# Optimization experiments

Measured on AMD Instinct MI355X. Metric: run time of the kernel, lower is better.

## Reference

```python
import jax, jax.numpy as jnp
import numpy as np

B, S, HID = 2, 2048, 4096
NH, D = 32, 128          # heads, head_dim
G, GS = 8, 4             # palu groups, group_size (heads per group)
RK = 256                 # rank per K group (rank_k[i])
RV = 2048                # total V rank
FGD = RV // G            # fused_group_dim = 256
FH = FGD * NH            # fused_hidden_dim = 8192
GD = HID // G            # k group_dim = 512
THETA = 10000.0


def setup_inputs() -> dict:
    key = jax.random.key(0)
    ks = jax.random.split(key, 7)
    hidden_states = jax.random.normal(ks[0], (B, S, HID), jnp.float32)
    causal = jnp.tril(jnp.ones((S, S), bool))
    attention_mask = jnp.broadcast_to(
        jnp.where(causal, 0.0, -1e9).astype(jnp.float32)[None, None], (B, 1, S, S))
    position_ids = jnp.broadcast_to(jnp.arange(S, dtype=jnp.int32)[None], (B, S))
    sc = 0.02
    Wq = sc * jax.random.normal(ks[1], (HID, HID), jnp.float32)
    WVT = sc * jax.random.normal(ks[2], (G * RK, HID), jnp.float32)   # k_proj.VT
    U = sc * jax.random.normal(ks[3], (GD, G * RK), jnp.float32)      # k_proj.U
    Wv = sc * jax.random.normal(ks[4], (RV, HID), jnp.float32)
    Wo = sc * jax.random.normal(ks[5], (HID, FH), jnp.float32)
    return dict(hidden_states=hidden_states, attention_mask=attention_mask,
                position_ids=position_ids, Wq=Wq, WVT=WVT, U=U, Wv=Wv, Wo=Wo)


def _rotate_half(x):
    return jnp.concatenate([-x[..., D // 2:], x[..., :D // 2]], axis=-1)


def reference(hidden_states, attention_mask, position_ids, Wq, WVT, U, Wv, Wo):
    b, q, _ = hidden_states.shape
    # projections
    qs = (hidden_states @ Wq.T).reshape(b, q, NH, D).transpose(0, 2, 1, 3)      # (b,H,q,d)
    k_lat = (hidden_states @ WVT.T).reshape(b, q, G, RK).transpose(0, 2, 1, 3)  # (b,G,q,RK)
    v_lat = (hidden_states @ Wv.T).reshape(b, q, G, FGD).transpose(0, 2, 1, 3)  # (b,G,q,FGD)
    # headwise reconstruction of K: group g latent (RK) -> group_dim (512) via U[:, g-slice]
    Ug = U.reshape(GD, G, RK)
    keys = jnp.einsum('bgsr,dgr->bgsd', k_lat, Ug)                 # (b,G,q,512)
    keys = keys.transpose(0, 2, 1, 3).reshape(b, q, NH, D).transpose(0, 2, 1, 3)  # (b,H,q,d)
    # RoPE
    inv_freq = 1.0 / (THETA ** (jnp.arange(0, D, 2, dtype=jnp.float32) / D))
    freqs = position_ids.astype(jnp.float32)[..., None] * inv_freq            # (b,q,d/2)
    emb = jnp.concatenate([freqs, freqs], axis=-1)
    cos, sin = jnp.cos(emb)[:, None], jnp.sin(emb)[:, None]                   # (b,1,q,d)
    qs = qs * cos + _rotate_half(qs) * sin
    keys = keys * cos + _rotate_half(keys) * sin
    # attention scores + mask + fp32 softmax
    attn = jnp.einsum('bhqd,bhkd->bhqk', qs, keys) / np.sqrt(D).astype(np.float32)
    attn = attn + attention_mask
    attn = jax.nn.softmax(attn.astype(jnp.float32), axis=-1).astype(qs.dtype)
    # PALU fused low-rank V path: exact torch reshape/transpose semantics
    aw = attn.reshape(b, G, q * GS, q)                                        # (b,G,gs*q,kv)
    out = jnp.einsum('bgik,bgkf->bgif', aw, v_lat)                            # (b,G,gs*q,FGD)
    out = out.transpose(0, 2, 1, 3).reshape(b, q, FH)                         # (b,q,8192)
    return out @ Wo.T
```

## Files before the change

### kernel.cpp

```cpp
#include <hip/hip_runtime.h>
#include <hip/hip_bf16.h>

typedef __hip_bfloat16 bf16;
typedef __bf16 bf16x8 __attribute__((ext_vector_type(8)));
typedef float f32x4 __attribute__((ext_vector_type(4)));

#define MFMA16(a, b, c) __builtin_amdgcn_mfma_f32_16x16x32_bf16(a, b, c, 0, 0, 0)

__device__ __forceinline__ void llds16(const bf16* g, bf16* lds) {
  __builtin_amdgcn_global_load_lds(
      (const __attribute__((address_space(1))) unsigned int*)g,
      (__attribute__((address_space(3))) unsigned int*)lds, 16, 0, 0);
}

__device__ __forceinline__ void storeC(float* p, float v) { *p = v; }
__device__ __forceinline__ void storeC(bf16* p, float v) { *p = __float2bfloat16(v); }

__global__ __launch_bounds__(256) void cvt_f2b(const float* __restrict__ in,
                                               bf16* __restrict__ out, int n4) {
  int i = blockIdx.x * 256 + threadIdx.x;
  if (i >= n4) return;
  float4 v = ((const float4*)in)[i];
  union { bf16 h[4]; short4 s; } u;
  u.h[0] = __float2bfloat16(v.x);
  u.h[1] = __float2bfloat16(v.y);
  u.h[2] = __float2bfloat16(v.z);
  u.h[3] = __float2bfloat16(v.w);
  ((short4*)out)[i] = u.s;
}

template <typename OUT_T>
__global__ __launch_bounds__(512, 2) void gemm256(
    const bf16* __restrict__ A, const bf16* __restrict__ B, OUT_T* __restrict__ C,
    int K, int lda, int ldb, int ldc) {
  extern __shared__ bf16 sm[];
  const int t = threadIdx.x, w = t >> 6, l = t & 63;
  const int lane_r = l & 15, quad = l >> 4;
  const int wm = (w >> 2) * 128, wn = (w & 3) * 64;
  const long m0 = (long)blockIdx.y * 256, n0 = (long)blockIdx.x * 256;
  const int r0 = t >> 2;
  const int c0 = (((t & 3) ^ (r0 & 3)) << 3);
  const bf16* As0 = A + (m0 + r0) * lda + c0;
  const bf16* As1 = A + (m0 + r0 + 128) * lda + c0;
  const bf16* Bs0 = B + (n0 + r0) * ldb + c0;
  const bf16* Bs1 = B + (n0 + r0 + 128) * ldb + c0;

#define STAGE(sl, kt)                                   \
  do {                                                  \
    long ko = (long)(kt) * 32;                          \
    bf16* dA = sm + (sl) * 16384;                       \
    bf16* dB = dA + 8192;                               \
    llds16(As0 + ko, dA + t * 8);                       \
    llds16(As1 + ko, dA + (t + 512) * 8);               \
    llds16(Bs0 + ko, dB + t * 8);                       \
    llds16(Bs1 + ko, dB + (t + 512) * 8);               \
  } while (0)

  f32x4 acc[8][4] = {};
  const int KT = K >> 5;
  const int sw = quad ^ (lane_r & 3);

  STAGE(0, 0);
  STAGE(1, 1);
  int sl = 0;
  for (int kt = 0; kt < KT; ++kt) {
    const int pre = KT - 1 - kt;
    if (pre >= 2) {
      int sl2 = sl + 2;
      if (sl2 >= 3) sl2 -= 3;
      STAGE(sl2, kt + 2);
      asm volatile("s_waitcnt vmcnt(8)" ::: "memory");
    } else if (pre == 1) {
      asm volatile("s_waitcnt vmcnt(4)" ::: "memory");
    } else {
      asm volatile("s_waitcnt vmcnt(0)" ::: "memory");
    }
    __builtin_amdgcn_s_barrier();
    __builtin_amdgcn_sched_barrier(0);
    const bf16* Al = sm + sl * 16384;
    const bf16* Bl = Al + 8192;
    bf16x8 af[8], bfr[4];
#pragma unroll
    for (int mt = 0; mt < 8; ++mt)
      af[mt] = *(const bf16x8*)&Al[(wm + mt * 16 + lane_r) * 32 + sw * 8];
#pragma unroll
    for (int nt = 0; nt < 4; ++nt)
      bfr[nt] = *(const bf16x8*)&Bl[(wn + nt * 16 + lane_r) * 32 + sw * 8];
    __builtin_amdgcn_s_setprio(1);
#pragma unroll
    for (int mt = 0; mt < 8; ++mt)
#pragma unroll
      for (int nt = 0; nt < 4; ++nt)
        acc[mt][nt] = MFMA16(af[mt], bfr[nt], acc[mt][nt]);
    __builtin_amdgcn_s_setprio(0);
    __builtin_amdgcn_s_barrier();
    if (++sl == 3) sl = 0;
  }
#undef STAGE

#pragma unroll
  for (int mt = 0; mt < 8; ++mt)
#pragma unroll
    for (int nt = 0; nt < 4; ++nt) {
      long row = m0 + wm + mt * 16 + quad * 4;
      long col = n0 + wn + nt * 16 + lane_r;
#pragma unroll
      for (int r = 0; r < 4; ++r) storeC(&C[(row + r) * ldc + col], acc[mt][nt][r]);
    }
}

template <typename OUT_T>
__global__ __launch_bounds__(256) void gemm_bt(
    const bf16* __restrict__ A, const bf16* __restrict__ B, OUT_T* __restrict__ C,
    int M, int N, int K, int lda, int ldb, int ldc,
    long batchA, long batchB, long batchC) {
  __shared__ alignas(16) bf16 As[128 * 32];
  __shared__ alignas(16) bf16 Bs[128 * 32];
  const int t = threadIdx.x;
  const int w = t >> 6, l = t & 63;
  const int lane_r = l & 15, quad = l >> 4;
  const int wm = (w >> 1) * 64, wn = (w & 1) * 64;
  const long m0 = (long)blockIdx.y * 128, n0 = (long)blockIdx.x * 128;
  A += (long)blockIdx.z * batchA;
  B += (long)blockIdx.z * batchB;
  C += (long)blockIdx.z * batchC;
  const int r0a = t >> 2;
  const int cba = (t & 3) * 8;
  f32x4 acc[4][4] = {};
  for (int k0 = 0; k0 < K; k0 += 32) {
    llds16(A + (m0 + r0a) * lda + k0 + cba, &As[t * 8]);
    llds16(A + (m0 + r0a + 64) * lda + k0 + cba, &As[(t + 256) * 8]);
    llds16(B + (n0 + r0a) * ldb + k0 + cba, &Bs[t * 8]);
    llds16(B + (n0 + r0a + 64) * ldb + k0 + cba, &Bs[(t + 256) * 8]);
    __syncthreads();
    bf16x8 af[4], bfr[4];
#pragma unroll
    for (int mt = 0; mt < 4; ++mt)
      af[mt] = *(const bf16x8*)&As[(wm + mt * 16 + lane_r) * 32 + quad * 8];
#pragma unroll
    for (int nt = 0; nt < 4; ++nt)
      bfr[nt] = *(const bf16x8*)&Bs[(wn + nt * 16 + lane_r) * 32 + quad * 8];
#pragma unroll
    for (int mt = 0; mt < 4; ++mt)
#pragma unroll
      for (int nt = 0; nt < 4; ++nt)
        acc[mt][nt] = MFMA16(af[mt], bfr[nt], acc[mt][nt]);
    __syncthreads();
  }
#pragma unroll
  for (int mt = 0; mt < 4; ++mt)
#pragma unroll
    for (int nt = 0; nt < 4; ++nt) {
      long row = m0 + wm + mt * 16 + quad * 4;
      long col = n0 + wn + nt * 16 + lane_r;
#pragma unroll
      for (int r = 0; r < 4; ++r) storeC(&C[(row + r) * ldc + col], acc[mt][nt][r]);
    }
}

__global__ __launch_bounds__(256) void rope_perm(const bf16* __restrict__ in, int ldin,
                                                 bf16* __restrict__ out,
                                                 const int* __restrict__ pos_ids) {
  int idx = blockIdx.x * 256 + threadIdx.x;
  int d = idx & 63;
  int h = (idx >> 6) & 31;
  int bs = idx >> 11;
  int b = bs >> 11, s = bs & 2047;
  float pos = (float)pos_ids[bs];
  float inv = exp2f(-(float)d * (13.287712379549449f / 64.0f));
  float fr = pos * inv, sn, cs;
  sincosf(fr, &sn, &cs);
  long bi = (long)bs * ldin + h * 128 + d;
  long bo = ((long)(b * 32 + h) * 2048 + s) * 128 + d;
  float x1 = __bfloat162float(in[bi]);
  float x2 = __bfloat162float(in[bi + 64]);
  out[bo] = __float2bfloat16(x1 * cs - x2 * sn);
  out[bo + 64] = __float2bfloat16(x2 * cs + x1 * sn);
}

__global__ __launch_bounds__(256) void transpose_kernel(const bf16* __restrict__ v,
                                                        int ldv,
                                                        bf16* __restrict__ vt) {
  __shared__ bf16 tile[32][33];
  int b = blockIdx.z;
  int c0 = blockIdx.x * 32;
  int r0 = blockIdx.y * 32;
  int tx = threadIdx.x & 31, ty = threadIdx.x >> 5;
#pragma unroll
  for (int p = 0; p < 4; ++p) {
    int r = ty + p * 8;
    tile[r][tx] = v[((long)b * 2048 + r0 + r) * ldv + c0 + tx];
  }
  __syncthreads();
#pragma unroll
  for (int p = 0; p < 4; ++p) {
    int cidx = ty + p * 8;
    int cg = c0 + cidx;
    int g = cg >> 8, d = cg & 255;
    int s = r0 + tx;
    vt[((long)((b * 8 + g) * 64 + (s >> 5))) * 8192 + d * 32 + (s & 31)] = tile[tx][cidx];
  }
}

__global__ __launch_bounds__(512, 2) void attn_kernel(const bf16* __restrict__ Q,
                                                      const bf16* __restrict__ Kg,
                                                      const bf16* __restrict__ Vt,
                                                      bf16* __restrict__ fused) {
  __shared__ alignas(16) bf16 smem[32768];
  const int t = threadIdx.x, w = t >> 6, l = t & 63;
  const int lane_r = l & 15, quad = l >> 4;
  const int L = blockIdx.x;
  const int half = L >> 8, pair = L & 255;
  const int hb = pair >> 2, slot = pair & 3;
  const int qt = half ? slot : (7 - slot);
  const int b = hb >> 5, h = hb & 31;
  const int g = h >> 2, j = h & 3;
  const int q0 = qt * 256;
  const int qr0 = q0 + w * 32;
  const float scale = 0.08838834764831845f;

  const bf16* qbase = Q + ((long)(b * 32 + h) * 2048 + qr0 + lane_r) * 128 + quad * 8;
  bf16x8 qf[2][4];
#pragma unroll
  for (int m = 0; m < 2; ++m)
#pragma unroll
    for (int kd = 0; kd < 4; ++kd)
      qf[m][kd] = *(const bf16x8*)(qbase + m * 2048 + kd * 32);

  f32x4 acc[2][16] = {};
  float m_i[2][4], l_i[2][4];
#pragma unroll
  for (int m = 0; m < 2; ++m)
#pragma unroll
    for (int r = 0; r < 4; ++r) { m_i[m][r] = -1e30f; l_i[m][r] = 0.f; }

  const bf16* Kbase = Kg + (long)(b * 32 + h) * 262144;
  const bf16* Vtg = Vt + (long)(b * 8 + g) * 524288;
  const int kr = t >> 4, ck = (t & 15) ^ (kr & 15);
  const bf16* ksrc = Kbase + kr * 128 + ck * 8;
  const int vrA = t >> 2, cvA = (t & 3) ^ (vrA & 3);
  const int vrB = (t + 512) >> 2, cvB = ((t + 512) & 3) ^ (vrB & 3);
  const bf16* vsrcA = Vtg + vrA * 32 + cvA * 8;
  const bf16* vsrcB = Vtg + vrB * 32 + cvB * 8;

#define STAGE_T(buf, kt)                                                    \
  do {                                                                      \
    llds16(ksrc + (long)(kt) * 4096, &smem[(buf) * 4096 + t * 8]);          \
    llds16(vsrcA + (long)(kt) * 8192, &smem[8192 + (buf) * 8192 + t * 8]);  \
    llds16(vsrcB + (long)(kt) * 8192,                                       \
           &smem[8192 + (buf) * 8192 + (t + 512) * 8]);                     \
  } while (0)

  bf16* Pw = smem + 24576 + w * 1024;
  const int pslot = quad ^ ((lane_r >> 1) & 3);
  const int vslot = quad ^ (lane_r & 3);
  int poff0[4], poff1[4];
  {
    const int hi = lane_r >> 3, lo = lane_r & 7;
#pragma unroll
    for (int r = 0; r < 4; ++r) {
      int rq = quad * 4 + r;
      int sw2 = (rq >> 1) & 3;
      poff0[r] = rq * 32 + ((hi ^ sw2) << 3) + lo;
      poff1[r] = rq * 32 + (((2 + hi) ^ sw2) << 3) + lo;
    }
  }

  const int nk = qt * 8 + 8;
  const int kwmax = qt * 8 + w;

  STAGE_T(0, 0);
  for (int kt = 0; kt < nk; ++kt) {
    if (kt + 1 < nk) {
      STAGE_T((kt + 1) & 1, kt + 1);
      asm volatile("s_waitcnt vmcnt(3)" ::: "memory");
    } else {
      asm volatile("s_waitcnt vmcnt(0)" ::: "memory");
    }
    __builtin_amdgcn_s_barrier();
    __builtin_amdgcn_sched_barrier(0);
    const bf16* Ks = &smem[(kt & 1) * 4096];
    const bf16* Vs = &smem[8192 + (kt & 1) * 8192];

    if (kt <= kwmax) {
      const int k0 = kt * 32;
      const bool diag = (kt == kwmax);
      f32x4 s[2][2] = {};
#pragma unroll
      for (int ks = 0; ks < 2; ++ks) {
        bf16x8 kf[4];
#pragma unroll
        for (int kd = 0; kd < 4; ++kd) {
          int csw = (kd * 4 + quad) ^ lane_r;
          kf[kd] = *(const bf16x8*)&Ks[(ks * 16 + lane_r) * 128 + csw * 8];
        }
#pragma unroll
        for (int kd = 0; kd < 4; ++kd) {
          s[0][ks] = MFMA16(qf[0][kd], kf[kd], s[0][ks]);
          s[1][ks] = MFMA16(qf[1][kd], kf[kd], s[1][ks]);
        }
      }
      float sc[2][2][4];
      if (diag) {
#pragma unroll
        for (int m = 0; m < 2; ++m) {
          const int qrowb = qr0 + m * 16 + quad * 4;
#pragma unroll
          for (int r = 0; r < 4; ++r) {
            sc[m][0][r] = (k0 + lane_r <= qrowb + r) ? s[m][0][r] * scale : -1e30f;
            sc[m][1][r] = (k0 + 16 + lane_r <= qrowb + r) ? s[m][1][r] * scale : -1e30f;
          }
        }
      } else {
#pragma unroll
        for (int m = 0; m < 2; ++m)
#pragma unroll
          for (int r = 0; r < 4; ++r) {
            sc[m][0][r] = s[m][0][r] * scale;
            sc[m][1][r] = s[m][1][r] * scale;
          }
      }

#pragma unroll
      for (int m = 0; m < 2; ++m) {
        float mx[4];
        bool grow = false;
#pragma unroll
        for (int r = 0; r < 4; ++r) {
          float v = fmaxf(sc[m][0][r], sc[m][1][r]);
#pragma unroll
          for (int o = 1; o < 16; o <<= 1) v = fmaxf(v, __shfl_xor(v, o));
          mx[r] = v;
          grow = grow || (v > m_i[m][r]);
        }
        if (__any((int)grow)) {
#pragma unroll
          for (int r = 0; r < 4; ++r) {
            float mnew = fmaxf(m_i[m][r], mx[r]);
            float alpha = __expf(m_i[m][r] - mnew);
            m_i[m][r] = mnew;
            l_i[m][r] *= alpha;
#pragma unroll
            for (int nt = 0; nt < 16; ++nt) acc[m][nt][r] *= alpha;
          }
        }
#pragma unroll
        for (int r = 0; r < 4; ++r) {
          float p0 = __expf(sc[m][0][r] - m_i[m][r]);
          float p1 = __expf(sc[m][1][r] - m_i[m][r]);
          float rs = p0 + p1;
#pragma unroll
          for (int o = 1; o < 16; o <<= 1) rs += __shfl_xor(rs, o);
          l_i[m][r] += rs;
          Pw[m * 512 + poff0[r]] = __float2bfloat16(p0);
          Pw[m * 512 + poff1[r]] = __float2bfloat16(p1);
        }
      }

      bf16x8 pf0 = *(const bf16x8*)&Pw[lane_r * 32 + pslot * 8];
      bf16x8 pf1 = *(const bf16x8*)&Pw[(16 + lane_r) * 32 + pslot * 8];
      __builtin_amdgcn_s_setprio(1);
#pragma unroll
      for (int nt = 0; nt < 16; ++nt) {
        bf16x8 vf = *(const bf16x8*)&Vs[(nt * 16 + lane_r) * 32 + vslot * 8];
        acc[0][nt] = MFMA16(pf0, vf, acc[0][nt]);
        acc[1][nt] = MFMA16(pf1, vf, acc[1][nt]);
      }
      __builtin_amdgcn_s_setprio(0);
    }
    __builtin_amdgcn_s_barrier();
  }
#undef STAGE_T

  __syncthreads();
  bf16* EP = smem + w * 4096;
#pragma unroll
  for (int m = 0; m < 2; ++m) {
#pragma unroll
    for (int r = 0; r < 4; ++r) {
      float inv = 1.0f / l_i[m][r];
#pragma unroll
      for (int nt = 0; nt < 16; ++nt)
        EP[(quad * 4 + r) * 256 + nt * 16 + lane_r] = __float2bfloat16(acc[m][nt][r] * inv);
    }
#pragma unroll
    for (int op = 0; op < 8; ++op) {
      int row = op * 2 + (l >> 5);
      int qrow = qr0 + m * 16 + row;
      int sOut = j * 512 + (qrow >> 2), fi = qrow & 3;
      bf16x8 vread = *(const bf16x8*)&EP[row * 256 + (l & 31) * 8];
      *(bf16x8*)(fused + ((long)(b * 2048 + sOut)) * 8192 + fi * 2048 + g * 256 +
                 (l & 31) * 8) = vread;
    }
  }
}

extern "C" void kernel_launch(void* const* d_in, const int* in_sizes, int n_in,
                              void* d_out, int out_size, void* d_ws, size_t ws_size,
                              hipStream_t stream) {
  const float* hidden = (const float*)d_in[0];
  const int* pos_ids = (const int*)d_in[2];
  const float* Wq = (const float*)d_in[3];
  const float* WVT = (const float*)d_in[4];
  const float* U = (const float*)d_in[5];
  const float* Wv = (const float*)d_in[6];
  const float* Wo = (const float*)d_in[7];
  float* out = (float*)d_out;

  bf16* ws = (bf16*)d_ws;
  bf16* WB = ws;
  bf16* UB = WB + 33554432;
  bf16* hidB = UB + 1048576;
  bf16* proj = hidB + 16777216;
  bf16* Kb = proj + 33554432;
  bf16* vtB = Kb + 16777216;
  bf16* fusedB = vtB + 8388608;
  bf16* Qh = hidB;
  bf16* Kh = proj;

  static bool attr_set = false;
  if (!attr_set) {
    hipFuncSetAttribute((const void*)gemm256<bf16>,
                        hipFuncAttributeMaxDynamicSharedMemorySize, 98304);
    hipFuncSetAttribute((const void*)gemm256<float>,
                        hipFuncAttributeMaxDynamicSharedMemorySize, 98304);
    attr_set = true;
  }

  cvt_f2b<<<16384, 256, 0, stream>>>(hidden, hidB, 4194304);
  cvt_f2b<<<16384, 256, 0, stream>>>(Wq, WB, 4194304);
  cvt_f2b<<<8192, 256, 0, stream>>>(WVT, WB + 16777216, 2097152);
  cvt_f2b<<<8192, 256, 0, stream>>>(Wv, WB + 25165824, 2097152);
  gemm256<bf16><<<dim3(32, 16), 512, 98304, stream>>>(hidB, WB, proj, 4096, 4096,
                                                      4096, 8192);
  cvt_f2b<<<1024, 256, 0, stream>>>(U, UB, 262144);
  gemm_bt<bf16><<<dim3(4, 32, 8), 256, 0, stream>>>(proj + 4096, UB, Kb, 4096, 512,
                                                    256, 8192, 2048, 4096, 256, 256,
                                                    512);
  transpose_kernel<<<dim3(64, 64, 2), 256, 0, stream>>>(proj + 6144, 8192, vtB);
  rope_perm<<<32768, 256, 0, stream>>>(proj, 8192, Qh, pos_ids);
  rope_perm<<<32768, 256, 0, stream>>>(Kb, 4096, Kh, pos_ids);
  cvt_f2b<<<32768, 256, 0, stream>>>(Wo, WB, 8388608);
  attn_kernel<<<dim3(512, 1, 1), 512, 0, stream>>>(Qh, Kh, vtB, fusedB);
  gemm256<float><<<dim3(16, 16), 512, 98304, stream>>>(fusedB, WB, out, 8192, 8192,
                                                       8192, 4096);
}
```

Measured before the change: 1.193 ms.

## Split GEMM k-step into two MFMA phases and change LDS swizzle

The 256x256 GEMM main loop now splits each k-step into two half-N MFMA phases, issuing the A-tile prefetch during the first phase and the B-tile prefetch during the second, with extra barriers and lgkmcnt waits. This interleaves global-to-LDS loads with compute instead of issuing all four loads up front. The LDS XOR swizzle in both the GEMM and the attention V tile changes from row&3 to (row>>1)&3 to cut bank conflicts on 16-byte reads. The extra barriers per k-step add synchronisation cost, and the finer prefetch split risks a race if the slot-reuse ordering is wrong.

```diff
diff --git a/kernel.cpp b/kernel.cpp
--- a/kernel.cpp
+++ b/kernel.cpp
@@ -39,64 +39,91 @@
   const int wm = (w >> 2) * 128, wn = (w & 3) * 64;
   const long m0 = (long)blockIdx.y * 256, n0 = (long)blockIdx.x * 256;
   const int r0 = t >> 2;
-  const int c0 = (((t & 3) ^ (r0 & 3)) << 3);
+  const int c0 = (((t & 3) ^ ((r0 >> 1) & 3)) << 3);
   const bf16* As0 = A + (m0 + r0) * lda + c0;
   const bf16* As1 = A + (m0 + r0 + 128) * lda + c0;
   const bf16* Bs0 = B + (n0 + r0) * ldb + c0;
   const bf16* Bs1 = B + (n0 + r0 + 128) * ldb + c0;
 
-#define STAGE(sl, kt)                                   \
-  do {                                                  \
-    long ko = (long)(kt) * 32;                          \
-    bf16* dA = sm + (sl) * 16384;                       \
-    bf16* dB = dA + 8192;                               \
-    llds16(As0 + ko, dA + t * 8);                       \
-    llds16(As1 + ko, dA + (t + 512) * 8);               \
-    llds16(Bs0 + ko, dB + t * 8);                       \
-    llds16(Bs1 + ko, dB + (t + 512) * 8);               \
+#define STAGE_A(sl_, kt_)                                \
+  do {                                                   \
+    long ko = (long)(kt_) * 32;                          \
+    bf16* dA = sm + (sl_) * 16384;                       \
+    llds16(As0 + ko, dA + t * 8);                        \
+    llds16(As1 + ko, dA + (t + 512) * 8);                \
+  } while (0)
+#define STAGE_B(sl_, kt_)                                \
+  do {                                                   \
+    long ko = (long)(kt_) * 32;                          \
+    bf16* dB = sm + (sl_) * 16384 + 8192;                \
+    llds16(Bs0 + ko, dB + t * 8);                        \
+    llds16(Bs1 + ko, dB + (t + 512) * 8);                \
   } while (0)
 
   f32x4 acc[8][4] = {};
   const int KT = K >> 5;
-  const int sw = quad ^ (lane_r & 3);
-
-  STAGE(0, 0);
-  STAGE(1, 1);
+  const int sw = quad ^ ((lane_r >> 1) & 3);
+
+  STAGE_A(0, 0);
+  STAGE_B(0, 0);
+  STAGE_A(1, 1);
+  STAGE_B(1, 1);
+  asm volatile("s_waitcnt vmcnt(4)" ::: "memory");
+  __builtin_amdgcn_s_barrier();
+
   int sl = 0;
   for (int kt = 0; kt < KT; ++kt) {
-    const int pre = KT - 1 - kt;
-    if (pre >= 2) {
-      int sl2 = sl + 2;
-      if (sl2 >= 3) sl2 -= 3;
-      STAGE(sl2, kt + 2);
-      asm volatile("s_waitcnt vmcnt(8)" ::: "memory");
-    } else if (pre == 1) {
+    const bf16* Al = sm + sl * 16384;
+    const bf16* Bl = Al + 8192;
+    int sl2 = sl + 2;
+    if (sl2 >= 3) sl2 -= 3;
+    const bool pf = (kt + 2 < KT);
+    bf16x8 af[8], bfr[2];
+#pragma unroll
+    for (int mt = 0; mt < 8; ++mt)
+      af[mt] = *(const bf16x8*)&Al[(wm + mt * 16 + lane_r) * 32 + sw * 8];
+#pragma unroll
+    for (int nt = 0; nt < 2; ++nt)
+      bfr[nt] = *(const bf16x8*)&Bl[(wn + nt * 16 + lane_r) * 32 + sw * 8];
+    if (pf) STAGE_A(sl2, kt + 2);
+    __builtin_amdgcn_sched_barrier(0);
+    __builtin_amdgcn_s_barrier();
+    asm volatile("s_waitcnt lgkmcnt(0)" ::: "memory");
+    __builtin_amdgcn_sched_barrier(0);
+    __builtin_amdgcn_s_setprio(1);
+#pragma unroll
+    for (int mt = 0; mt < 8; ++mt) {
+      acc[mt][0] = MFMA16(af[mt], bfr[0], acc[mt][0]);
+      acc[mt][1] = MFMA16(af[mt], bfr[1], acc[mt][1]);
+    }
+    __builtin_amdgcn_s_setprio(0);
+    __builtin_amdgcn_s_barrier();
+    bf16x8 bfr2[2];
+#pragma unroll
+    for (int nt = 0; nt < 2; ++nt)
+      bfr2[nt] = *(const bf16x8*)&Bl[(wn + (nt + 2) * 16 + lane_r) * 32 + sw * 8];
+    if (pf) {
+      STAGE_B(sl2, kt + 2);
       asm volatile("s_waitcnt vmcnt(4)" ::: "memory");
     } else {
       asm volatile("s_waitcnt vmcnt(0)" ::: "memory");
     }
-    __builtin_amdgcn_s_barrier();
     __builtin_amdgcn_sched_barrier(0);
-    const bf16* Al = sm + sl * 16384;
-    const bf16* Bl = Al + 8192;
-    bf16x8 af[8], bfr[4];
-#pragma unroll
-    for (int mt = 0; mt < 8; ++mt)
-      af[mt] = *(const bf16x8*)&Al[(wm + mt * 16 + lane_r) * 32 + sw * 8];
-#pragma unroll
-    for (int nt = 0; nt < 4; ++nt)
-      bfr[nt] = *(const bf16x8*)&Bl[(wn + nt * 16 + lane_r) * 32 + sw * 8];
+    __builtin_amdgcn_s_barrier();
+    asm volatile("s_waitcnt lgkmcnt(0)" ::: "memory");
+    __builtin_amdgcn_sched_barrier(0);
     __builtin_amdgcn_s_setprio(1);
 #pragma unroll
-    for (int mt = 0; mt < 8; ++mt)
-#pragma unroll
-      for (int nt = 0; nt < 4; ++nt)
-        acc[mt][nt] = MFMA16(af[mt], bfr[nt], acc[mt][nt]);
+    for (int mt = 0; mt < 8; ++mt) {
+      acc[mt][2] = MFMA16(af[mt], bfr2[0], acc[mt][2]);
+      acc[mt][3] = MFMA16(af[mt], bfr2[1], acc[mt][3]);
+    }
     __builtin_amdgcn_s_setprio(0);
     __builtin_amdgcn_s_barrier();
     if (++sl == 3) sl = 0;
   }
-#undef STAGE
+#undef STAGE_A
+#undef STAGE_B
 
 #pragma unroll
   for (int mt = 0; mt < 8; ++mt)
@@ -238,8 +265,8 @@
   const bf16* Vtg = Vt + (long)(b * 8 + g) * 524288;
   const int kr = t >> 4, ck = (t & 15) ^ (kr & 15);
   const bf16* ksrc = Kbase + kr * 128 + ck * 8;
-  const int vrA = t >> 2, cvA = (t & 3) ^ (vrA & 3);
-  const int vrB = (t + 512) >> 2, cvB = ((t + 512) & 3) ^ (vrB & 3);
+  const int vrA = t >> 2, cvA = (t & 3) ^ ((vrA >> 1) & 3);
+  const int vrB = (t + 512) >> 2, cvB = (t & 3) ^ ((vrB >> 1) & 3);
   const bf16* vsrcA = Vtg + vrA * 32 + cvA * 8;
   const bf16* vsrcB = Vtg + vrB * 32 + cvB * 8;
 
@@ -253,7 +280,7 @@
 
   bf16* Pw = smem + 24576 + w * 1024;
   const int pslot = quad ^ ((lane_r >> 1) & 3);
-  const int vslot = quad ^ (lane_r & 3);
+  const int vslot = quad ^ ((lane_r >> 1) & 3);
   int poff0[4], poff1[4];
   {
     const int hi = lane_r >> 3, lo = lane_r & 7;
```

After: 1.162 ms. 1.03x faster.
